# Kernel optimization log

Measured on AMD Instinct MI355X. Metric: run time of the kernel, lower is better.

The kernel has to match this reference:

```python
import jax, jax.numpy as jnp
import numpy as np

M, K, V, A = 50, 50, 200, 64  # memory_size, key_dim, value_dim, attention_dim
B, S = 512, 1024


def setup_inputs() -> dict:
    key = jax.random.key(0)
    ks = jax.random.split(key, 12)
    kaiming = lambda k, shape, fan_in: jax.random.normal(k, shape, jnp.float32) * np.sqrt(2.0 / fan_in)
    return {
        "query_embeddings": jax.random.normal(ks[0], (B, S, K), jnp.float32),
        "attention_features": jax.random.normal(ks[1], (B, S, A), jnp.float32),
        "value_memory": jax.random.normal(ks[2], (B, M, V), jnp.float32),
        "key_memory": kaiming(ks[3], (M, K), K),
        "Wc": kaiming(ks[4], (K, K), K),   # correlation_projection
        "bc": jnp.zeros((K,), jnp.float32),
        "Wr": kaiming(ks[5], (A, V), V),   # guided_read_projection
        "br": jnp.zeros((A,), jnp.float32),
        "We": kaiming(ks[6], (V, 2 * A), 2 * A),  # erase_gate
        "be": jnp.zeros((V,), jnp.float32),
        "Wa": kaiming(ks[7], (V, 2 * A), 2 * A),  # add_gate
        "ba": jnp.zeros((V,), jnp.float32),
    }


def reference(query_embeddings, attention_features, value_memory,
              key_memory, Wc, bc, Wr, br, We, be, Wa, ba):
    # update_memory=True path: sequential DKVMN read/erase/add over time.

    def read(mem, q_t, a_t):
        ck = jnp.tanh(q_t @ Wc.T + bc)                     # [B,K]
        w = jax.nn.softmax(ck @ key_memory.T, axis=-1)     # [B,M]
        rc = jnp.einsum('bm,bmv->bv', w, mem) @ Wr.T + br  # [B,A]
        return w, rc

    def write(mem, w, a_t, rc):
        wi = jnp.concatenate([a_t, rc], axis=-1)           # [B,2A]
        erase = jax.nn.sigmoid(wi @ We.T + be)             # [B,V]
        add = jnp.tanh(wi @ Wa.T + ba)                     # [B,V]
        w3 = w[:, :, None]
        return mem * (1.0 - w3 * erase[:, None, :]) + w3 * add[:, None, :]

    def step(mem, xs):
        q_t, a_t = xs
        w, rc = read(mem, q_t, a_t)
        return write(mem, w, a_t, rc), (rc, w)

    # first S-1 steps update memory; last step reads only
    q_seq = jnp.swapaxes(query_embeddings[:, :-1], 0, 1)   # [S-1,B,K]
    a_seq = jnp.swapaxes(attention_features[:, :-1], 0, 1)
    mem_final, (rcs, ws) = jax.lax.scan(step, value_memory, (q_seq, a_seq))
    w_last, rc_last = read(mem_final, query_embeddings[:, -1], attention_features[:, -1])

    read_content = jnp.concatenate([jnp.swapaxes(rcs, 0, 1), rc_last[:, None]], axis=1)  # [B,S,A]
    memory_weights = jnp.concatenate([jnp.swapaxes(ws, 0, 1), w_last[:, None]], axis=1)  # [B,S,M]
    return read_content, mem_final, memory_weights
```

## Files before the change

### kernel.cpp

```cpp
#include <hip/hip_runtime.h>
#include <stdint.h>

#define Md 50
#define Kd 50
#define Vd 200
#define Ad 64
#define Bd 512
#define Sd 1024

__device__ __forceinline__ float fast_tanh(float x) {
    float e = __expf(2.f * x);
    return 1.f - 2.f / (e + 1.f);
}

__device__ __forceinline__ float sigmoidf_(float x) {
    return 1.f / (1.f + __expf(-x));
}

__device__ __forceinline__ float rl(float v, int l) {
    return __uint_as_float((unsigned)__builtin_amdgcn_readlane((int)__float_as_uint(v), l));
}

__global__ __launch_bounds__(512, 2)
void agm_kernel(const float* __restrict__ q_in,
                const float* __restrict__ a_in,
                const float* __restrict__ mem_in,
                const float* __restrict__ key_in,
                const float* __restrict__ Wc_in,
                const float* __restrict__ bc_in,
                const float* __restrict__ Wr_in,
                const float* __restrict__ br_in,
                const float* __restrict__ We_in,
                const float* __restrict__ be_in,
                const float* __restrict__ Wa_in,
                const float* __restrict__ ba_in,
                float* __restrict__ rc_out,
                float* __restrict__ mem_out,
                float* __restrict__ w_out)
{
    __shared__ float sWcT[Kd * Kd];
    __shared__ float sKeyT[Kd * Md];
    __shared__ __align__(16) float sWrT[Vd * 66];
    __shared__ float sbc[Kd], sbr[Ad], sbe[Vd], sba[Vd];
    __shared__ float sq[2][2][Kd];
    __shared__ float sw[2][2][64];
    __shared__ __align__(16) float swi[2][128];
    __shared__ __align__(16) float srcvI[Vd * 2];
    __shared__ float spe[2][2][Vd];
    __shared__ float spa[2][2][Vd];

    const int tid = threadIdx.x;
    const int blk = blockIdx.x;
    const int hb  = tid >> 8;
    const int mv  = tid & 255;
    const int wv  = tid >> 6;
    const int ln  = tid & 63;
    const int bidx = blk * 2 + hb;

    for (int idx = tid; idx < Kd * Kd; idx += 512) {
        int i = idx / Kd, k = idx % Kd;
        sWcT[k * Kd + i]  = Wc_in[idx];
        sKeyT[k * Md + i] = key_in[idx];
    }
    for (int idx = tid; idx < Ad * Vd; idx += 512) {
        int a = idx / Vd, v = idx % Vd;
        sWrT[v * 66 + a] = Wr_in[idx];
    }
    if (tid < Kd) sbc[tid] = bc_in[tid];
    if (tid < Ad) sbr[tid] = br_in[tid];
    if (tid < Vd) { sbe[tid] = be_in[tid]; sba[tid] = ba_in[tid]; }

    const int wh5 = wv >> 2;
    const int r5  = (wv & 3) * 50 + ln;
    float WeC[64], WaC[64];
    if (ln < 50) {
        const float4* wep = (const float4*)(We_in + (size_t)r5 * 128 + wh5 * 64);
        const float4* wap = (const float4*)(Wa_in + (size_t)r5 * 128 + wh5 * 64);
        #pragma unroll
        for (int c = 0; c < 16; ++c) {
            float4 ue = wep[c], ua = wap[c];
            WeC[4*c+0]=ue.x; WeC[4*c+1]=ue.y; WeC[4*c+2]=ue.z; WeC[4*c+3]=ue.w;
            WaC[4*c+0]=ua.x; WaC[4*c+1]=ua.y; WaC[4*c+2]=ua.z; WaC[4*c+3]=ua.w;
        }
    } else {
        #pragma unroll
        for (int j = 0; j < 64; ++j) { WeC[j] = 0.f; WaC[j] = 0.f; }
    }

    const int g4 = (tid >> 3) & 31;
    const int c4 = tid & 7;

    float memcol[Md];
    if (mv < Vd) {
        #pragma unroll
        for (int m = 0; m < Md; ++m)
            memcol[m] = mem_in[(size_t)bidx * Md * Vd + m * Vd + mv];
    } else {
        #pragma unroll
        for (int m = 0; m < Md; ++m) memcol[m] = 0.f;
    }

    const bool is_q = (tid < 100);
    const int qhb = tid / 50, qk = tid % 50;
    const bool is_a = (tid >= 256 && tid < 384);
    const int ahb = (tid - 256) >> 6, aj = tid & 63;

    auto fused_s1s2 = [&](int par, int h) {
        float ckv = 0.f;
        if (ln < Kd) {
            float acc = sbc[ln];
            #pragma unroll
            for (int k = 0; k < Kd; ++k)
                acc = fmaf(sq[par][h][k], sWcT[k * Kd + ln], acc);
            ckv = fast_tanh(acc);
        }
        float lg = -1e30f;
        if (ln < Md) {
            float l0 = 0.f, l1 = 0.f;
            #pragma unroll
            for (int k = 0; k < Kd; k += 2) {
                l0 = fmaf(rl(ckv, k),     sKeyT[k * Md + ln],       l0);
                l1 = fmaf(rl(ckv, k + 1), sKeyT[(k + 1) * Md + ln], l1);
            }
            lg = l0 + l1;
        }
        float mx = lg;
        #pragma unroll
        for (int off = 32; off > 0; off >>= 1)
            mx = fmaxf(mx, __shfl_xor(mx, off));
        float e = (ln < Md) ? __expf(lg - mx) : 0.f;
        float sm = e;
        #pragma unroll
        for (int off = 32; off > 0; off >>= 1)
            sm += __shfl_xor(sm, off);
        if (ln < Md) sw[par][h][ln] = e / sm;
    };

    auto s5dot = [&](int xoff, int whi) {
        float xA = swi[0][xoff + ln];
        float xB = swi[1][xoff + ln];
        float pe0 = 0.f, pa0 = 0.f, pe1 = 0.f, pa1 = 0.f;
        #pragma unroll
        for (int j = 0; j < 64; ++j) {
            float sa = rl(xA, j);
            float sb = rl(xB, j);
            pe0 = fmaf(sa, WeC[j], pe0);
            pa0 = fmaf(sa, WaC[j], pa0);
            pe1 = fmaf(sb, WeC[j], pe1);
            pa1 = fmaf(sb, WaC[j], pa1);
        }
        if (ln < 50) {
            spe[whi][0][r5] = pe0; spe[whi][1][r5] = pe1;
            spa[whi][0][r5] = pa0; spa[whi][1][r5] = pa1;
        }
    };

    if (is_q) {
        sq[0][qhb][qk] = q_in[(size_t)(blk*2+qhb) * Sd * Kd + qk];
        sq[1][qhb][qk] = q_in[(size_t)(blk*2+qhb) * Sd * Kd + Kd + qk];
    }
    if (is_a) swi[ahb][aj] = a_in[(size_t)(blk*2+ahb) * Sd * Ad + aj];
    __syncthreads();

    if (wv == 2 || wv == 3) fused_s1s2(0, wv - 2);

    float qreg = 0.f, areg = 0.f;
    if (is_q) qreg = q_in[(size_t)(blk*2+qhb) * Sd * Kd + 2 * Kd + qk];
    if (is_a) areg = a_in[(size_t)(blk*2+ahb) * Sd * Ad + Ad + aj];
    __syncthreads();

    float swreg = sw[0][hb][ln];
    if (mv < Vd) {
        float p0 = 0.f, p1 = 0.f;
        #pragma unroll
        for (int m = 0; m < Md; m += 2) {
            p0 = fmaf(rl(swreg, m),     memcol[m],     p0);
            p1 = fmaf(rl(swreg, m + 1), memcol[m + 1], p1);
        }
        srcvI[mv * 2 + hb] = p0 + p1;
    }
    if (mv < Md) w_out[(size_t)bidx * Sd * Md + mv] = swreg;

    for (int t = 0; t < Sd; ++t) {
        __syncthreads();

        if (wv >= 4) {
            float q00 = 0.f, q01 = 0.f, q10 = 0.f, q11 = 0.f;
            #pragma unroll
            for (int j = 0; j < 25; ++j) {
                int v = c4 * 25 + j;
                float2 sv = *(const float2*)&srcvI[v * 2];
                float2 wr = *(const float2*)&sWrT[v * 66 + 2 * g4];
                q00 = fmaf(sv.x, wr.x, q00);
                q01 = fmaf(sv.y, wr.x, q01);
                q10 = fmaf(sv.x, wr.y, q10);
                q11 = fmaf(sv.y, wr.y, q11);
            }
            #pragma unroll
            for (int off = 1; off < 8; off <<= 1) {
                q00 += __shfl_xor(q00, off);
                q01 += __shfl_xor(q01, off);
                q10 += __shfl_xor(q10, off);
                q11 += __shfl_xor(q11, off);
            }
            if (c4 == 0) {
                int a0 = 2 * g4, a1 = a0 + 1;
                float rc00 = q00 + sbr[a0], rc01 = q01 + sbr[a0];
                float rc10 = q10 + sbr[a1], rc11 = q11 + sbr[a1];
                swi[0][64 + a0] = rc00; swi[1][64 + a0] = rc01;
                swi[0][64 + a1] = rc10; swi[1][64 + a1] = rc11;
                size_t o0 = (size_t)(blk*2+0) * Sd * Ad + (size_t)t * Ad;
                size_t o1 = (size_t)(blk*2+1) * Sd * Ad + (size_t)t * Ad;
                rc_out[o0 + a0] = rc00; rc_out[o1 + a0] = rc01;
                rc_out[o0 + a1] = rc10; rc_out[o1 + a1] = rc11;
            }
        } else if (t < Sd - 1) {
            s5dot(0, 0);
        }
        __syncthreads();

        if (t == Sd - 1) break;

        if (wv >= 4) {
            s5dot(64, 1);
        } else if (wv >= 2) {
            fused_s1s2((t + 1) & 1, wv - 2);
        }
        __syncthreads();

        if (mv < Vd) {
            float ev = sigmoidf_(spe[0][hb][mv] + spe[1][hb][mv] + sbe[mv]);
            float av = fast_tanh(spa[0][hb][mv] + spa[1][hb][mv] + sba[mv]);
            #pragma unroll
            for (int m = 0; m < Md; ++m) {
                float wm = rl(swreg, m);
                memcol[m] = fmaf(wm, fmaf(-ev, memcol[m], av), memcol[m]);
            }
        }
        if (is_a) swi[ahb][aj] = areg;
        if (is_q && t + 2 < Sd) sq[(t + 2) & 1][qhb][qk] = qreg;
        if (is_a && t + 2 < Sd)
            areg = a_in[(size_t)(blk*2+ahb) * Sd * Ad + (size_t)(t + 2) * Ad + aj];
        if (is_q && t + 3 < Sd)
            qreg = q_in[(size_t)(blk*2+qhb) * Sd * Kd + (size_t)(t + 3) * Kd + qk];
        swreg = sw[(t + 1) & 1][hb][ln];
        if (mv < Vd) {
            float p0 = 0.f, p1 = 0.f;
            #pragma unroll
            for (int m = 0; m < Md; m += 2) {
                p0 = fmaf(rl(swreg, m),     memcol[m],     p0);
                p1 = fmaf(rl(swreg, m + 1), memcol[m + 1], p1);
            }
            srcvI[mv * 2 + hb] = p0 + p1;
        }
        if (mv < Md)
            w_out[(size_t)bidx * Sd * Md + (size_t)(t + 1) * Md + mv] = swreg;
    }

    if (mv < Vd) {
        #pragma unroll
        for (int m = 0; m < Md; ++m)
            mem_out[(size_t)bidx * Md * Vd + m * Vd + mv] = memcol[m];
    }
}

extern "C" void kernel_launch(void* const* d_in, const int* in_sizes, int n_in,
                              void* d_out, int out_size, void* d_ws, size_t ws_size,
                              hipStream_t stream) {
    const float* q   = (const float*)d_in[0];
    const float* a   = (const float*)d_in[1];
    const float* mem = (const float*)d_in[2];
    const float* key = (const float*)d_in[3];
    const float* Wc  = (const float*)d_in[4];
    const float* bc  = (const float*)d_in[5];
    const float* Wr  = (const float*)d_in[6];
    const float* br  = (const float*)d_in[7];
    const float* We  = (const float*)d_in[8];
    const float* be  = (const float*)d_in[9];
    const float* Wa  = (const float*)d_in[10];
    const float* ba  = (const float*)d_in[11];

    float* out = (float*)d_out;
    float* rc_out  = out;
    float* mem_out = rc_out + (size_t)Bd * Sd * Ad;
    float* w_out   = mem_out + (size_t)Bd * Md * Vd;

    hipLaunchKernelGGL(agm_kernel, dim3(256), dim3(512), 0, stream,
                       q, a, mem, key, Wc, bc, Wr, br, We, be, Wa, ba,
                       rc_out, mem_out, w_out);
}
```

Baseline: 5.920 ms.

## Precompute attention weights in a separate parallel kernel, restructure recurrent loop

The weights w do not depend on memory, so they are now computed for all batches and time steps by a separate, fully parallel kernel and written straight to the output. The recurrent kernel reads w from global memory with prefetch instead of running the correlation projection and softmax each step. It also fuses the memory update with the next step's read, and spreads the erase/add gate dot products across 400 threads using vectorised LDS reads instead of readlane broadcasts. This shortens the serial per-step critical path, at the cost of an extra kernel launch and a global round-trip for w.

```diff
diff --git a/kernel.cpp b/kernel.cpp
--- a/kernel.cpp
+++ b/kernel.cpp
@@ -17,63 +17,127 @@
     return 1.f / (1.f + __expf(-x));
 }
 
-__device__ __forceinline__ float rl(float v, int l) {
-    return __uint_as_float((unsigned)__builtin_amdgcn_readlane((int)__float_as_uint(v), l));
+__global__ __launch_bounds__(256)
+void wpre_kernel(const float* __restrict__ q_in,
+                 const float* __restrict__ key_in,
+                 const float* __restrict__ Wc_in,
+                 const float* __restrict__ bc_in,
+                 float* __restrict__ w_out)
+{
+    __shared__ float sWc[Kd * 51];
+    __shared__ float sKey[Md * 51];
+    __shared__ float sbc[Kd];
+    __shared__ __align__(16) float sbuf[4][64];
+
+    const int tid = threadIdx.x;
+    for (int idx = tid; idx < Kd * Kd; idx += 256) {
+        int i = idx / Kd, j = idx % Kd;
+        sWc[i * 51 + j]  = Wc_in[idx];
+        sKey[i * 51 + j] = key_in[idx];
+    }
+    if (tid < Kd) sbc[tid] = bc_in[tid];
+    __syncthreads();
+
+    const int wv = tid >> 6, ln = tid & 63;
+    const int gw = blockIdx.x * 4 + wv;
+
+    for (int r = 0; r < 64; ++r) {
+        const size_t row = (size_t)gw * 64 + r;
+        float qv = 0.f;
+        if (ln < Kd) qv = q_in[row * Kd + ln];
+        sbuf[wv][ln] = qv;
+        __syncthreads();
+
+        float ck = 0.f;
+        if (ln < Kd) {
+            const float4* qp = (const float4*)sbuf[wv];
+            float acc = sbc[ln];
+            #pragma unroll
+            for (int c = 0; c < 12; ++c) {
+                float4 x = qp[c];
+                acc = fmaf(x.x, sWc[ln * 51 + 4 * c + 0], acc);
+                acc = fmaf(x.y, sWc[ln * 51 + 4 * c + 1], acc);
+                acc = fmaf(x.z, sWc[ln * 51 + 4 * c + 2], acc);
+                acc = fmaf(x.w, sWc[ln * 51 + 4 * c + 3], acc);
+            }
+            float2 x2 = *(const float2*)&sbuf[wv][48];
+            acc = fmaf(x2.x, sWc[ln * 51 + 48], acc);
+            acc = fmaf(x2.y, sWc[ln * 51 + 49], acc);
+            ck = fast_tanh(acc);
+        }
+        __syncthreads();
+        sbuf[wv][ln] = ck;
+        __syncthreads();
+
+        float lg = -1e30f;
+        if (ln < Md) {
+            const float4* cp = (const float4*)sbuf[wv];
+            float acc = 0.f;
+            #pragma unroll
+            for (int c = 0; c < 12; ++c) {
+                float4 x = cp[c];
+                acc = fmaf(x.x, sKey[ln * 51 + 4 * c + 0], acc);
+                acc = fmaf(x.y, sKey[ln * 51 + 4 * c + 1], acc);
+                acc = fmaf(x.z, sKey[ln * 51 + 4 * c + 2], acc);
+                acc = fmaf(x.w, sKey[ln * 51 + 4 * c + 3], acc);
+            }
+            float2 x2 = *(const float2*)&sbuf[wv][48];
+            acc = fmaf(x2.x, sKey[ln * 51 + 48], acc);
+            acc = fmaf(x2.y, sKey[ln * 51 + 49], acc);
+            lg = acc;
+        }
+        float mx = lg;
+        #pragma unroll
+        for (int off = 32; off > 0; off >>= 1)
+            mx = fmaxf(mx, __shfl_xor(mx, off));
+        float e = (ln < Md) ? __expf(lg - mx) : 0.f;
+        float sm = e;
+        #pragma unroll
+        for (int off = 32; off > 0; off >>= 1)
+            sm += __shfl_xor(sm, off);
+        if (ln < Md) w_out[row * Md + ln] = e / sm;
+        __syncthreads();
+    }
 }
 
 __global__ __launch_bounds__(512, 2)
-void agm_kernel(const float* __restrict__ q_in,
-                const float* __restrict__ a_in,
+void agm_kernel(const float* __restrict__ a_in,
                 const float* __restrict__ mem_in,
-                const float* __restrict__ key_in,
-                const float* __restrict__ Wc_in,
-                const float* __restrict__ bc_in,
                 const float* __restrict__ Wr_in,
                 const float* __restrict__ br_in,
                 const float* __restrict__ We_in,
                 const float* __restrict__ be_in,
                 const float* __restrict__ Wa_in,
                 const float* __restrict__ ba_in,
+                const float* __restrict__ w_in,
                 float* __restrict__ rc_out,
-                float* __restrict__ mem_out,
-                float* __restrict__ w_out)
+                float* __restrict__ mem_out)
 {
-    __shared__ float sWcT[Kd * Kd];
-    __shared__ float sKeyT[Kd * Md];
-    __shared__ __align__(16) float sWrT[Vd * 66];
-    __shared__ float sbc[Kd], sbr[Ad], sbe[Vd], sba[Vd];
-    __shared__ float sq[2][2][Kd];
-    __shared__ float sw[2][2][64];
+    __shared__ float sWrT[Vd * 66];
+    __shared__ float sbr[Ad];
     __shared__ __align__(16) float swi[2][128];
-    __shared__ __align__(16) float srcvI[Vd * 2];
+    __shared__ __align__(16) float sw[2][2][64];
     __shared__ float spe[2][2][Vd];
     __shared__ float spa[2][2][Vd];
+    __shared__ __align__(8) float srcvI[Vd * 2];
 
     const int tid = threadIdx.x;
     const int blk = blockIdx.x;
     const int hb  = tid >> 8;
     const int mv  = tid & 255;
-    const int wv  = tid >> 6;
-    const int ln  = tid & 63;
     const int bidx = blk * 2 + hb;
 
-    for (int idx = tid; idx < Kd * Kd; idx += 512) {
-        int i = idx / Kd, k = idx % Kd;
-        sWcT[k * Kd + i]  = Wc_in[idx];
-        sKeyT[k * Md + i] = key_in[idx];
-    }
     for (int idx = tid; idx < Ad * Vd; idx += 512) {
         int a = idx / Vd, v = idx % Vd;
         sWrT[v * 66 + a] = Wr_in[idx];
     }
-    if (tid < Kd) sbc[tid] = bc_in[tid];
     if (tid < Ad) sbr[tid] = br_in[tid];
-    if (tid < Vd) { sbe[tid] = be_in[tid]; sba[tid] = ba_in[tid]; }
-
-    const int wh5 = wv >> 2;
-    const int r5  = (wv & 3) * 50 + ln;
+
+    const bool isW = (tid < 400);
+    const int r5  = tid % 200;
+    const int wh5 = tid / 200;
     float WeC[64], WaC[64];
-    if (ln < 50) {
+    if (isW) {
         const float4* wep = (const float4*)(We_in + (size_t)r5 * 128 + wh5 * 64);
         const float4* wap = (const float4*)(Wa_in + (size_t)r5 * 128 + wh5 * 64);
         #pragma unroll
@@ -87,177 +151,163 @@
         for (int j = 0; j < 64; ++j) { WeC[j] = 0.f; WaC[j] = 0.f; }
     }
 
+    const bool isM = (mv < Vd);
+    float memcol[Md];
+    float ebias = 0.f, abias = 0.f;
+    if (isM) {
+        #pragma unroll
+        for (int m = 0; m < Md; ++m)
+            memcol[m] = mem_in[(size_t)bidx * Md * Vd + m * Vd + mv];
+        ebias = be_in[mv];
+        abias = ba_in[mv];
+    } else {
+        #pragma unroll
+        for (int m = 0; m < Md; ++m) memcol[m] = 0.f;
+    }
+
     const int g4 = (tid >> 3) & 31;
     const int c4 = tid & 7;
 
-    float memcol[Md];
-    if (mv < Vd) {
-        #pragma unroll
-        for (int m = 0; m < Md; ++m)
-            memcol[m] = mem_in[(size_t)bidx * Md * Vd + m * Vd + mv];
-    } else {
-        #pragma unroll
-        for (int m = 0; m < Md; ++m) memcol[m] = 0.f;
-    }
-
-    const bool is_q = (tid < 100);
-    const int qhb = tid / 50, qk = tid % 50;
-    const bool is_a = (tid >= 256 && tid < 384);
-    const int ahb = (tid - 256) >> 6, aj = tid & 63;
-
-    auto fused_s1s2 = [&](int par, int h) {
-        float ckv = 0.f;
-        if (ln < Kd) {
-            float acc = sbc[ln];
+    const bool isA = (tid < 128);
+    const int ahb = tid >> 6, aj = tid & 63;
+    const bool isWw = (tid >= 128 && tid < 228);
+    const int whb = (tid - 128) / 50, wm = (tid - 128) % 50;
+
+    auto s4_phase = [&](int tt) {
+        float q00 = 0.f, q01 = 0.f, q10 = 0.f, q11 = 0.f;
+        #pragma unroll
+        for (int j = 0; j < 25; ++j) {
+            int v = c4 * 25 + j;
+            float2 sv = *(const float2*)&srcvI[v * 2];
+            float2 wr = *(const float2*)&sWrT[v * 66 + 2 * g4];
+            q00 = fmaf(sv.x, wr.x, q00);
+            q01 = fmaf(sv.y, wr.x, q01);
+            q10 = fmaf(sv.x, wr.y, q10);
+            q11 = fmaf(sv.y, wr.y, q11);
+        }
+        #pragma unroll
+        for (int off = 1; off < 8; off <<= 1) {
+            q00 += __shfl_xor(q00, off);
+            q01 += __shfl_xor(q01, off);
+            q10 += __shfl_xor(q10, off);
+            q11 += __shfl_xor(q11, off);
+        }
+        if (c4 == 0) {
+            int a0 = 2 * g4, a1 = a0 + 1;
+            float rc00 = q00 + sbr[a0], rc01 = q01 + sbr[a0];
+            float rc10 = q10 + sbr[a1], rc11 = q11 + sbr[a1];
+            swi[0][64 + a0] = rc00; swi[1][64 + a0] = rc01;
+            swi[0][64 + a1] = rc10; swi[1][64 + a1] = rc11;
+            size_t o0 = ((size_t)(blk * 2 + 0) * Sd + tt) * Ad;
+            size_t o1 = ((size_t)(blk * 2 + 1) * Sd + tt) * Ad;
+            rc_out[o0 + a0] = rc00; rc_out[o1 + a0] = rc01;
+            rc_out[o0 + a1] = rc10; rc_out[o1 + a1] = rc11;
+        }
+    };
+
+    if (tid < 100) {
+        int b = tid / 50, m = tid % 50;
+        sw[0][b][m] = w_in[((size_t)(blk * 2 + b) * Sd + 0) * Md + m];
+        sw[1][b][m] = w_in[((size_t)(blk * 2 + b) * Sd + 1) * Md + m];
+    }
+    if (isA) swi[ahb][aj] = a_in[((size_t)(blk * 2 + ahb) * Sd + 0) * Ad + aj];
+    float areg = 0.f, wreg = 0.f;
+    if (isA) areg = a_in[((size_t)(blk * 2 + ahb) * Sd + 1) * Ad + aj];
+    if (isWw) wreg = w_in[((size_t)(blk * 2 + whb) * Sd + 2) * Md + wm];
+    __syncthreads();
+
+    if (isM) {
+        const float4* w0p = (const float4*)sw[0][hb];
+        float rv0 = 0.f, rv1 = 0.f;
+        #pragma unroll
+        for (int c = 0; c < 12; ++c) {
+            float4 wa = w0p[c];
+            rv0 = fmaf(wa.x, memcol[4*c+0], rv0);
+            rv1 = fmaf(wa.y, memcol[4*c+1], rv1);
+            rv0 = fmaf(wa.z, memcol[4*c+2], rv0);
+            rv1 = fmaf(wa.w, memcol[4*c+3], rv1);
+        }
+        float2 wa2 = *(const float2*)&sw[0][hb][48];
+        rv0 = fmaf(wa2.x, memcol[48], rv0);
+        rv1 = fmaf(wa2.y, memcol[49], rv1);
+        srcvI[mv * 2 + hb] = rv0 + rv1;
+    }
+    __syncthreads();
+    if (tid >= 256) s4_phase(0);
+    __syncthreads();
+
+    for (int t = 0; t < Sd - 1; ++t) {
+        if (isW) {
+            const float4* x0p = (const float4*)&swi[0][wh5 * 64];
+            const float4* x1p = (const float4*)&swi[1][wh5 * 64];
+            float pe0 = 0.f, pa0 = 0.f, pe1 = 0.f, pa1 = 0.f;
             #pragma unroll
-            for (int k = 0; k < Kd; ++k)
-                acc = fmaf(sq[par][h][k], sWcT[k * Kd + ln], acc);
-            ckv = fast_tanh(acc);
-        }
-        float lg = -1e30f;
-        if (ln < Md) {
-            float l0 = 0.f, l1 = 0.f;
+            for (int c = 0; c < 16; ++c) {
+                float4 x0 = x0p[c];
+                float4 x1 = x1p[c];
+                float w0 = WeC[4*c+0], w1 = WeC[4*c+1], w2 = WeC[4*c+2], w3 = WeC[4*c+3];
+                float u0 = WaC[4*c+0], u1 = WaC[4*c+1], u2 = WaC[4*c+2], u3 = WaC[4*c+3];
+                pe0 = fmaf(x0.x, w0, pe0); pe0 = fmaf(x0.y, w1, pe0);
+                pe0 = fmaf(x0.z, w2, pe0); pe0 = fmaf(x0.w, w3, pe0);
+                pa0 = fmaf(x0.x, u0, pa0); pa0 = fmaf(x0.y, u1, pa0);
+                pa0 = fmaf(x0.z, u2, pa0); pa0 = fmaf(x0.w, u3, pa0);
+                pe1 = fmaf(x1.x, w0, pe1); pe1 = fmaf(x1.y, w1, pe1);
+                pe1 = fmaf(x1.z, w2, pe1); pe1 = fmaf(x1.w, w3, pe1);
+                pa1 = fmaf(x1.x, u0, pa1); pa1 = fmaf(x1.y, u1, pa1);
+                pa1 = fmaf(x1.z, u2, pa1); pa1 = fmaf(x1.w, u3, pa1);
+            }
+            spe[wh5][0][r5] = pe0; spe[wh5][1][r5] = pe1;
+            spa[wh5][0][r5] = pa0; spa[wh5][1][r5] = pa1;
+        }
+        __syncthreads();
+
+        if (isM) {
+            float se_ = spe[0][hb][mv] + spe[1][hb][mv] + ebias;
+            float sa_ = spa[0][hb][mv] + spa[1][hb][mv] + abias;
+            float ev = sigmoidf_(se_);
+            float av = fast_tanh(sa_);
+            const float4* w0p = (const float4*)sw[t & 1][hb];
+            const float4* w1p = (const float4*)sw[(t + 1) & 1][hb];
+            float rv0 = 0.f, rv1 = 0.f;
             #pragma unroll
-            for (int k = 0; k < Kd; k += 2) {
-                l0 = fmaf(rl(ckv, k),     sKeyT[k * Md + ln],       l0);
-                l1 = fmaf(rl(ckv, k + 1), sKeyT[(k + 1) * Md + ln], l1);
-            }
-            lg = l0 + l1;
-        }
-        float mx = lg;
-        #pragma unroll
-        for (int off = 32; off > 0; off >>= 1)
-            mx = fmaxf(mx, __shfl_xor(mx, off));
-        float e = (ln < Md) ? __expf(lg - mx) : 0.f;
-        float sm = e;
-        #pragma unroll
-        for (int off = 32; off > 0; off >>= 1)
-            sm += __shfl_xor(sm, off);
-        if (ln < Md) sw[par][h][ln] = e / sm;
-    };
-
-    auto s5dot = [&](int xoff, int whi) {
-        float xA = swi[0][xoff + ln];
-        float xB = swi[1][xoff + ln];
-        float pe0 = 0.f, pa0 = 0.f, pe1 = 0.f, pa1 = 0.f;
-        #pragma unroll
-        for (int j = 0; j < 64; ++j) {
-            float sa = rl(xA, j);
-            float sb = rl(xB, j);
-            pe0 = fmaf(sa, WeC[j], pe0);
-            pa0 = fmaf(sa, WaC[j], pa0);
-            pe1 = fmaf(sb, WeC[j], pe1);
-            pa1 = fmaf(sb, WaC[j], pa1);
-        }
-        if (ln < 50) {
-            spe[whi][0][r5] = pe0; spe[whi][1][r5] = pe1;
-            spa[whi][0][r5] = pa0; spa[whi][1][r5] = pa1;
-        }
-    };
-
-    if (is_q) {
-        sq[0][qhb][qk] = q_in[(size_t)(blk*2+qhb) * Sd * Kd + qk];
-        sq[1][qhb][qk] = q_in[(size_t)(blk*2+qhb) * Sd * Kd + Kd + qk];
-    }
-    if (is_a) swi[ahb][aj] = a_in[(size_t)(blk*2+ahb) * Sd * Ad + aj];
-    __syncthreads();
-
-    if (wv == 2 || wv == 3) fused_s1s2(0, wv - 2);
-
-    float qreg = 0.f, areg = 0.f;
-    if (is_q) qreg = q_in[(size_t)(blk*2+qhb) * Sd * Kd + 2 * Kd + qk];
-    if (is_a) areg = a_in[(size_t)(blk*2+ahb) * Sd * Ad + Ad + aj];
-    __syncthreads();
-
-    float swreg = sw[0][hb][ln];
-    if (mv < Vd) {
-        float p0 = 0.f, p1 = 0.f;
-        #pragma unroll
-        for (int m = 0; m < Md; m += 2) {
-            p0 = fmaf(rl(swreg, m),     memcol[m],     p0);
-            p1 = fmaf(rl(swreg, m + 1), memcol[m + 1], p1);
-        }
-        srcvI[mv * 2 + hb] = p0 + p1;
-    }
-    if (mv < Md) w_out[(size_t)bidx * Sd * Md + mv] = swreg;
-
-    for (int t = 0; t < Sd; ++t) {
-        __syncthreads();
-
-        if (wv >= 4) {
-            float q00 = 0.f, q01 = 0.f, q10 = 0.f, q11 = 0.f;
-            #pragma unroll
-            for (int j = 0; j < 25; ++j) {
-                int v = c4 * 25 + j;
-                float2 sv = *(const float2*)&srcvI[v * 2];
-                float2 wr = *(const float2*)&sWrT[v * 66 + 2 * g4];
-                q00 = fmaf(sv.x, wr.x, q00);
-                q01 = fmaf(sv.y, wr.x, q01);
-                q10 = fmaf(sv.x, wr.y, q10);
-                q11 = fmaf(sv.y, wr.y, q11);
-            }
-            #pragma unroll
-            for (int off = 1; off < 8; off <<= 1) {
-                q00 += __shfl_xor(q00, off);
-                q01 += __shfl_xor(q01, off);
-                q10 += __shfl_xor(q10, off);
-                q11 += __shfl_xor(q11, off);
-            }
-            if (c4 == 0) {
-                int a0 = 2 * g4, a1 = a0 + 1;
-                float rc00 = q00 + sbr[a0], rc01 = q01 + sbr[a0];
-                float rc10 = q10 + sbr[a1], rc11 = q11 + sbr[a1];
-                swi[0][64 + a0] = rc00; swi[1][64 + a0] = rc01;
-                swi[0][64 + a1] = rc10; swi[1][64 + a1] = rc11;
-                size_t o0 = (size_t)(blk*2+0) * Sd * Ad + (size_t)t * Ad;
-                size_t o1 = (size_t)(blk*2+1) * Sd * Ad + (size_t)t * Ad;
-                rc_out[o0 + a0] = rc00; rc_out[o1 + a0] = rc01;
-                rc_out[o0 + a1] = rc10; rc_out[o1 + a1] = rc11;
-            }
-        } else if (t < Sd - 1) {
-            s5dot(0, 0);
-        }
-        __syncthreads();
-
-        if (t == Sd - 1) break;
-
-        if (wv >= 4) {
-            s5dot(64, 1);
-        } else if (wv >= 2) {
-            fused_s1s2((t + 1) & 1, wv - 2);
-        }
-        __syncthreads();
-
-        if (mv < Vd) {
-            float ev = sigmoidf_(spe[0][hb][mv] + spe[1][hb][mv] + sbe[mv]);
-            float av = fast_tanh(spa[0][hb][mv] + spa[1][hb][mv] + sba[mv]);
-            #pragma unroll
-            for (int m = 0; m < Md; ++m) {
-                float wm = rl(swreg, m);
-                memcol[m] = fmaf(wm, fmaf(-ev, memcol[m], av), memcol[m]);
-            }
-        }
-        if (is_a) swi[ahb][aj] = areg;
-        if (is_q && t + 2 < Sd) sq[(t + 2) & 1][qhb][qk] = qreg;
-        if (is_a && t + 2 < Sd)
-            areg = a_in[(size_t)(blk*2+ahb) * Sd * Ad + (size_t)(t + 2) * Ad + aj];
-        if (is_q && t + 3 < Sd)
-            qreg = q_in[(size_t)(blk*2+qhb) * Sd * Kd + (size_t)(t + 3) * Kd + qk];
-        swreg = sw[(t + 1) & 1][hb][ln];
-        if (mv < Vd) {
-            float p0 = 0.f, p1 = 0.f;
-            #pragma unroll
-            for (int m = 0; m < Md; m += 2) {
-                p0 = fmaf(rl(swreg, m),     memcol[m],     p0);
-                p1 = fmaf(rl(swreg, m + 1), memcol[m + 1], p1);
-            }
-            srcvI[mv * 2 + hb] = p0 + p1;
-        }
-        if (mv < Md)
-            w_out[(size_t)bidx * Sd * Md + (size_t)(t + 1) * Md + mv] = swreg;
-    }
-
-    if (mv < Vd) {
+            for (int c = 0; c < 12; ++c) {
+                float4 wa = w0p[c];
+                float4 wb = w1p[c];
+                { float mc = memcol[4*c+0]; mc = fmaf(wa.x, fmaf(-ev, mc, av), mc);
+                  memcol[4*c+0] = mc; rv0 = fmaf(wb.x, mc, rv0); }
+                { float mc = memcol[4*c+1]; mc = fmaf(wa.y, fmaf(-ev, mc, av), mc);
+                  memcol[4*c+1] = mc; rv1 = fmaf(wb.y, mc, rv1); }
+                { float mc = memcol[4*c+2]; mc = fmaf(wa.z, fmaf(-ev, mc, av), mc);
+                  memcol[4*c+2] = mc; rv0 = fmaf(wb.z, mc, rv0); }
+                { float mc = memcol[4*c+3]; mc = fmaf(wa.w, fmaf(-ev, mc, av), mc);
+                  memcol[4*c+3] = mc; rv1 = fmaf(wb.w, mc, rv1); }
+            }
+            {
+                float2 wa2 = *(const float2*)&sw[t & 1][hb][48];
+                float2 wb2 = *(const float2*)&sw[(t + 1) & 1][hb][48];
+                { float mc = memcol[48]; mc = fmaf(wa2.x, fmaf(-ev, mc, av), mc);
+                  memcol[48] = mc; rv0 = fmaf(wb2.x, mc, rv0); }
+                { float mc = memcol[49]; mc = fmaf(wa2.y, fmaf(-ev, mc, av), mc);
+                  memcol[49] = mc; rv1 = fmaf(wb2.y, mc, rv1); }
+            }
+            srcvI[mv * 2 + hb] = rv0 + rv1;
+        }
+        __syncthreads();
+
+        if (tid >= 256) {
+            s4_phase(t + 1);
+        } else {
+            if (isA) swi[ahb][aj] = areg;
+            if (isWw && t + 2 < Sd) sw[t & 1][whb][wm] = wreg;
+        }
+        if (isA && t + 2 < Sd)
+            areg = a_in[((size_t)(blk * 2 + ahb) * Sd + (t + 2)) * Ad + aj];
+        if (isWw && t + 3 < Sd)
+            wreg = w_in[((size_t)(blk * 2 + whb) * Sd + (t + 3)) * Md + wm];
+        __syncthreads();
+    }
+
+    if (isM) {
         #pragma unroll
         for (int m = 0; m < Md; ++m)
             mem_out[(size_t)bidx * Md * Vd + m * Vd + mv] = memcol[m];
@@ -285,7 +335,9 @@
     float* mem_out = rc_out + (size_t)Bd * Sd * Ad;
     float* w_out   = mem_out + (size_t)Bd * Md * Vd;
 
+    hipLaunchKernelGGL(wpre_kernel, dim3(2048), dim3(256), 0, stream,
+                       q, key, Wc, bc, w_out);
     hipLaunchKernelGGL(agm_kernel, dim3(256), dim3(512), 0, stream,
-                       q, a, mem, key, Wc, bc, Wr, br, We, be, Wa, ba,
-                       rc_out, mem_out, w_out);
-}
+                       a, mem, Wr, br, We, be, Wa, ba, w_out,
+                       rc_out, mem_out);
+}
```

Result: faster. 5.746 ms (-3.0%).
